# Kernel tuning notes

Hardware: AMD Instinct MI355X
Metric: run time of the kernel (lower is better)

Reference implementation:

```python
import jax, jax.numpy as jnp
import numpy as np

N, E, D = 50000, 800000, 128

def setup_inputs() -> dict:
    key = jax.random.key(0)
    ks = jax.random.split(key, 8)
    s = 0.02
    x = jax.random.normal(ks[0], (N, D), dtype=jnp.float32)
    edge_index = jax.random.randint(ks[1], (2, E), 0, N, dtype=jnp.int64)
    Wn = jax.random.normal(ks[2], (D, D), dtype=jnp.float32) * s
    bn = jax.random.normal(ks[3], (D,), dtype=jnp.float32) * s
    We = jax.random.normal(ks[4], (D, 2 * D), dtype=jnp.float32) * s
    be = jax.random.normal(ks[5], (D,), dtype=jnp.float32) * s
    Wu = jax.random.normal(ks[6], (D, 3 * D), dtype=jnp.float32) * s
    bu = jax.random.normal(ks[7], (D,), dtype=jnp.float32) * s
    return {"x": x, "edge_index": edge_index, "Wn": Wn, "bn": bn,
            "We": We, "be": be, "Wu": Wu, "bu": bu}

def reference(x, edge_index, Wn, bn, We, be, Wu, bu):
    n = x.shape[0]
    # 1. per-node linear transform (torch Linear: x @ W.T + b)
    node = x @ Wn.T + bn                                   # [N, D]
    src, dst = edge_index[0], edge_index[1]
    # 2. per-edge embedding from concatenated endpoint node embeddings
    edge_in = jnp.concatenate([node[src], node[dst]], axis=1)  # [E, 2D]
    edge_emb = edge_in @ We.T + be                          # [E, D]
    # 3. scatter-sum neighbor node embeddings and incident edge embeddings to src vertex
    nbr_sum = jax.ops.segment_sum(node[dst], src, num_segments=n)    # [N, D]
    edge_sum = jax.ops.segment_sum(edge_emb, src, num_segments=n)   # [N, D]
    pre_gelu = jnp.concatenate([node, nbr_sum, edge_sum], axis=1)    # [N, 3D]
    # 4-5. GELU (exact, matching torch nn.GELU default) + final linear
    out = jax.nn.gelu(pre_gelu, approximate=False) @ Wu.T + bu       # [N, D]
    return out
```

## Files before the change

### kernel.cpp

```cpp
#include <hip/hip_runtime.h>
#include <hip/hip_bf16.h>
#include <math.h>

typedef __attribute__((ext_vector_type(8))) short short8;
typedef __attribute__((ext_vector_type(4))) float f32x4;

#define CAP8 16

__device__ __forceinline__ float bf2f(unsigned short u) {
    union { unsigned int i; float f; } c; c.i = ((unsigned int)u) << 16; return c.f;
}
__device__ __forceinline__ unsigned short f2bf(float f) {
    __hip_bfloat16 h = __float2bfloat16(f);
    union { __hip_bfloat16 h; unsigned short u; } c; c.h = h; return c.u;
}
__device__ __forceinline__ float gelu_exact(float x) {
    return 0.5f * x * (1.0f + erff(x * 0.7071067811865475f));
}
__device__ __forceinline__ short8 ldcvt8(const float* p) {
    float4 f0 = *(const float4*)p;
    float4 f1 = *(const float4*)(p + 4);
    short8 a;
    a[0] = (short)f2bf(f0.x); a[1] = (short)f2bf(f0.y);
    a[2] = (short)f2bf(f0.z); a[3] = (short)f2bf(f0.w);
    a[4] = (short)f2bf(f1.x); a[5] = (short)f2bf(f1.y);
    a[6] = (short)f2bf(f1.z); a[7] = (short)f2bf(f1.w);
    return a;
}
__device__ __forceinline__ int swz(int row, int colbyte) {
    return row * 256 + (colbyte ^ ((row & 7) << 4));
}

__device__ __forceinline__ int detect_flag(const int* ei, int E) {
    int orv = 0;
    int lim = (E < 64) ? E : 64;
    for (int i = 0; i < lim; i++) orv |= ei[2 * i + 1];
    return (orv == 0) ? 1 : 0;
}
__device__ __forceinline__ int ld_src(const int* ei, int flag, int E, int e) {
    return flag ? ei[2 * (size_t)e] : ei[e];
}
__device__ __forceinline__ int ld_dst(const int* ei, int flag, int E, int e) {
    return flag ? ei[2 * (size_t)(E + e)] : ei[E + e];
}

__device__ __forceinline__ void gemm1_body(int bid,
                                           const float* __restrict__ x,
                                           const float* __restrict__ Wn,
                                           const float* __restrict__ bias,
                                           unsigned short* __restrict__ node,
                                           unsigned short* __restrict__ Apre0,
                                           int N) {
    const int v0 = bid * 64;
    const int wave = threadIdx.x >> 6;
    const int lane = threadIdx.x & 63;
    const int m    = lane & 15;
    const int kq   = lane >> 4;

    short8 B[2][4];
#pragma unroll
    for (int ntl = 0; ntl < 2; ntl++) {
        const int j = (wave * 2 + ntl) * 16 + m;
#pragma unroll
        for (int kb = 0; kb < 4; kb++)
            B[ntl][kb] = ldcvt8(Wn + (size_t)j * 128 + kb * 32 + kq * 8);
    }

    f32x4 acc[4][2];
#pragma unroll
    for (int mt = 0; mt < 4; mt++)
#pragma unroll
        for (int ntl = 0; ntl < 2; ntl++) acc[mt][ntl] = (f32x4){0.f,0.f,0.f,0.f};

#pragma unroll
    for (int kb = 0; kb < 4; kb++) {
#pragma unroll
        for (int mt = 0; mt < 4; mt++) {
            const int row = v0 + mt * 16 + m;
            short8 a = (short8){0,0,0,0,0,0,0,0};
            if (row < N) a = ldcvt8(x + (size_t)row * 128 + kb * 32 + kq * 8);
#pragma unroll
            for (int ntl = 0; ntl < 2; ntl++)
                acc[mt][ntl] = __builtin_amdgcn_mfma_f32_16x16x32_bf16(a, B[ntl][kb], acc[mt][ntl], 0, 0, 0);
        }
    }

    const int ocol = lane & 15;
#pragma unroll
    for (int mt = 0; mt < 4; mt++) {
#pragma unroll
        for (int ntl = 0; ntl < 2; ntl++) {
            const int col = (wave * 2 + ntl) * 16 + ocol;
            const float bval = bias[col];
#pragma unroll
            for (int r = 0; r < 4; r++) {
                const int row = v0 + mt * 16 + (lane >> 4) * 4 + r;
                if (row < N) {
                    const float v = acc[mt][ntl][r] + bval;
                    node[(size_t)row * 128 + col]  = f2bf(v);
                    Apre0[(size_t)row * 128 + col] = f2bf(gelu_exact(v));
                }
            }
        }
    }
}

__launch_bounds__(256)
__global__ void fused_a(const float* __restrict__ x,
                        const float* __restrict__ Wn,
                        const float* __restrict__ bn,
                        unsigned short* __restrict__ node,
                        unsigned short* __restrict__ Apre0,
                        const int* __restrict__ ei,
                        int* __restrict__ cursor8,
                        unsigned short* __restrict__ csr8,
                        int E, int N, int mblocks) {
    const int grp = blockIdx.x >> 3;
    if ((grp % 5) == 2) {
        const int mid = ((grp - 2) / 5) * 8 + (int)(blockIdx.x & 7);
        if (mid < mblocks) gemm1_body(mid, x, Wn, bn, node, Apre0, N);
        return;
    }
    __shared__ int sflag;
    if (threadIdx.x == 0) sflag = detect_flag(ei, E);
    __syncthreads();
    const int fgrp = grp - (grp + 2) / 5;
    const int e = (fgrp * 8 + (int)(blockIdx.x & 7)) * 256 + (int)threadIdx.x;
    if (e >= E) return;
    const int s = ld_src(ei, sflag, E, e);
    const int d = ld_dst(ei, sflag, E, e);
    if ((unsigned)s >= (unsigned)N || (unsigned)d >= (unsigned)N) return;
    const int b = (int)(blockIdx.x & 7);
    const int p = atomicAdd(&cursor8[(size_t)b * N + s], 1);
    if (p < CAP8) csr8[(size_t)s * 128 + b * CAP8 + p] = (unsigned short)d;
}

__launch_bounds__(256)
__global__ void gather_kernel(const int* __restrict__ cursor8,
                              const unsigned short* __restrict__ csr8,
                              const unsigned short* __restrict__ node,
                              unsigned short* __restrict__ nbr,
                              unsigned short* __restrict__ gnbr,
                              int N) {
    __shared__ int degB[8][8];
    const int v0 = blockIdx.x * 8;
    const int tid = threadIdx.x;
    if (tid < 64) {
        const int b = tid >> 3, vi = tid & 7;
        const int v = v0 + vi;
        int c = (v < N) ? cursor8[(size_t)b * N + v] : 0;
        degB[vi][b] = (c > CAP8) ? CAP8 : c;
    }
    __syncthreads();

    const int vl = tid >> 5;
    const int p  = (tid >> 4) & 1;
    const int c  = (tid & 15) * 8;
    const int v  = v0 + vl;

    float acc[8] = {0.f,0.f,0.f,0.f,0.f,0.f,0.f,0.f};
    if (v < N) {
        const unsigned short* __restrict__ vbase = csr8 + (size_t)v * 128;
#pragma unroll
        for (int bi = 0; bi < 4; bi++) {
            const int b = bi * 2 + p;
            const int cnt = degB[vl][b];
            const unsigned short* base = vbase + b * CAP8;
            int j = 0;
            for (; j + 2 <= cnt; j += 2) {
                const int i0 = base[j], i1 = base[j + 1];
                short8 a0 = *(const short8*)(node + (size_t)i0 * 128 + c);
                short8 a1 = *(const short8*)(node + (size_t)i1 * 128 + c);
#pragma unroll
                for (int k = 0; k < 8; k++)
                    acc[k] += bf2f((unsigned short)a0[k]) + bf2f((unsigned short)a1[k]);
            }
            if (j < cnt) {
                const int i0 = base[j];
                short8 a0 = *(const short8*)(node + (size_t)i0 * 128 + c);
#pragma unroll
                for (int k = 0; k < 8; k++) acc[k] += bf2f((unsigned short)a0[k]);
            }
        }
    }
#pragma unroll
    for (int k = 0; k < 8; k++) acc[k] += __shfl_xor(acc[k], 16);

    if (v < N) {
        short8 o;
        if (p == 0) {
#pragma unroll
            for (int k = 0; k < 8; k++) o[k] = (short)f2bf(acc[k]);
            *(short8*)(nbr + (size_t)v * 128 + c) = o;
        } else {
#pragma unroll
            for (int k = 0; k < 8; k++) o[k] = (short)f2bf(gelu_exact(acc[k]));
            *(short8*)(gnbr + (size_t)v * 128 + c) = o;
        }
    }
}

__launch_bounds__(256)
__global__ void gemm23_kernel(const int* __restrict__ cursor8,
                              const unsigned short* __restrict__ node,
                              const unsigned short* __restrict__ nbr,
                              const unsigned short* __restrict__ gnbr,
                              const unsigned short* __restrict__ Apre0,
                              const float* __restrict__ We,
                              const float* __restrict__ be,
                              const float* __restrict__ Wu,
                              const float* __restrict__ bu,
                              float* __restrict__ out, int N) {
    __shared__ unsigned short p2T[64 * 128];
    __shared__ float degT[64];

    const int v0   = blockIdx.x * 64;
    const int tid  = threadIdx.x;
    const int wave = tid >> 6;
    const int lane = tid & 63;
    const int m    = lane & 15;
    const int kq   = lane >> 4;

    if (tid < 64) {
        const int v = v0 + tid;
        int s = 0;
        if (v < N) {
#pragma unroll
            for (int b = 0; b < 8; b++) {
                int c = cursor8[(size_t)b * N + v];
                s += (c > CAP8) ? CAP8 : c;
            }
        }
        degT[tid] = (float)s;
    }
    __syncthreads();

    {
        short8 B[2][4][2];
#pragma unroll
        for (int ntl = 0; ntl < 2; ntl++) {
            const int j = (wave * 2 + ntl) * 16 + m;
#pragma unroll
            for (int kb = 0; kb < 4; kb++)
#pragma unroll
                for (int s = 0; s < 2; s++)
                    B[ntl][kb][s] = ldcvt8(We + (size_t)j * 256 + s * 128 + kb * 32 + kq * 8);
        }

        f32x4 acc2[4][2];
#pragma unroll
        for (int mt = 0; mt < 4; mt++)
#pragma unroll
            for (int ntl = 0; ntl < 2; ntl++) acc2[mt][ntl] = (f32x4){0.f,0.f,0.f,0.f};

#pragma unroll
        for (int kb = 0; kb < 4; kb++) {
#pragma unroll
            for (int mt = 0; mt < 4; mt++) {
                const int lrow = mt * 16 + m;
                const int row  = v0 + lrow;
                short8 an = (short8){0,0,0,0,0,0,0,0};
                short8 ab = an;
                if (row < N) {
                    an = *(const short8*)(node + (size_t)row * 128 + kb * 32 + kq * 8);
                    ab = *(const short8*)(nbr  + (size_t)row * 128 + kb * 32 + kq * 8);
                    const float dg = degT[lrow];
#pragma unroll
                    for (int k = 0; k < 8; k++)
                        an[k] = (short)f2bf(dg * bf2f((unsigned short)an[k]));
                }
#pragma unroll
                for (int ntl = 0; ntl < 2; ntl++) {
                    acc2[mt][ntl] = __builtin_amdgcn_mfma_f32_16x16x32_bf16(an, B[ntl][kb][0], acc2[mt][ntl], 0, 0, 0);
                    acc2[mt][ntl] = __builtin_amdgcn_mfma_f32_16x16x32_bf16(ab, B[ntl][kb][1], acc2[mt][ntl], 0, 0, 0);
                }
            }
        }

        const int ocol = lane & 15;
#pragma unroll
        for (int mt = 0; mt < 4; mt++) {
#pragma unroll
            for (int ntl = 0; ntl < 2; ntl++) {
                const int col = (wave * 2 + ntl) * 16 + ocol;
                const float bval = be[col];
#pragma unroll
                for (int r = 0; r < 4; r++) {
                    const int lrow = mt * 16 + (lane >> 4) * 4 + r;
                    const float dg = degT[lrow];
                    const float vv = gelu_exact(acc2[mt][ntl][r] + dg * bval);
                    *(unsigned short*)((char*)p2T + swz(lrow, col * 2)) = f2bf(vv);
                }
            }
        }
    }
    __syncthreads();

    {
        f32x4 acc3[4][2];
#pragma unroll
        for (int mt = 0; mt < 4; mt++)
#pragma unroll
            for (int ntl = 0; ntl < 2; ntl++) acc3[mt][ntl] = (f32x4){0.f,0.f,0.f,0.f};

#pragma unroll
        for (int s = 0; s < 3; s++) {
            short8 B3[2][4];
#pragma unroll
            for (int ntl = 0; ntl < 2; ntl++) {
                const int j = (wave * 2 + ntl) * 16 + m;
#pragma unroll
                for (int kb = 0; kb < 4; kb++)
                    B3[ntl][kb] = ldcvt8(Wu + (size_t)j * 384 + s * 128 + kb * 32 + kq * 8);
            }
#pragma unroll
            for (int kb = 0; kb < 4; kb++) {
#pragma unroll
                for (int mt = 0; mt < 4; mt++) {
                    const int lrow = mt * 16 + m;
                    const int row  = v0 + lrow;
                    short8 a = (short8){0,0,0,0,0,0,0,0};
                    if (s == 0) {
                        if (row < N) a = *(const short8*)(Apre0 + (size_t)row * 128 + kb * 32 + kq * 8);
                    } else if (s == 1) {
                        if (row < N) a = *(const short8*)(gnbr + (size_t)row * 128 + kb * 32 + kq * 8);
                    } else {
                        a = *(const short8*)((const char*)p2T + swz(lrow, kb * 64 + kq * 16));
                    }
#pragma unroll
                    for (int ntl = 0; ntl < 2; ntl++)
                        acc3[mt][ntl] = __builtin_amdgcn_mfma_f32_16x16x32_bf16(a, B3[ntl][kb], acc3[mt][ntl], 0, 0, 0);
                }
            }
        }

        const int ocol = lane & 15;
#pragma unroll
        for (int mt = 0; mt < 4; mt++) {
#pragma unroll
            for (int ntl = 0; ntl < 2; ntl++) {
                const int col = (wave * 2 + ntl) * 16 + ocol;
                const float bval = bu[col];
#pragma unroll
                for (int r = 0; r < 4; r++) {
                    const int row = v0 + mt * 16 + (lane >> 4) * 4 + r;
                    if (row < N)
                        out[(size_t)row * 128 + col] = acc3[mt][ntl][r] + bval;
                }
            }
        }
    }
}

extern "C" void kernel_launch(void* const* d_in, const int* in_sizes, int n_in,
                              void* d_out, int out_size, void* d_ws, size_t ws_size,
                              hipStream_t stream) {
    const float* x  = (const float*)d_in[0];
    const int*   ei = (const int*)d_in[1];
    const float* Wn = (const float*)d_in[2];
    const float* bn = (const float*)d_in[3];
    const float* We = (const float*)d_in[4];
    const float* be = (const float*)d_in[5];
    const float* Wu = (const float*)d_in[6];
    const float* bu = (const float*)d_in[7];

    const int N = in_sizes[0] / 128;
    const int E = in_sizes[1] / 2;

    char* ws = (char*)d_ws;
    size_t off = 0;
    unsigned short* node  = (unsigned short*)(ws + off); off += (size_t)N * 128 * 2;
    unsigned short* Apre0 = (unsigned short*)(ws + off); off += (size_t)N * 128 * 2;
    unsigned short* nbr   = (unsigned short*)(ws + off); off += (size_t)N * 128 * 2;
    unsigned short* gnbr  = (unsigned short*)(ws + off); off += (size_t)N * 128 * 2;
    off = (off + 255) & ~(size_t)255;
    int* cursor8 = (int*)(ws + off);                     off += (size_t)8 * N * 4;
    off = (off + 255) & ~(size_t)255;
    unsigned short* csr8 = (unsigned short*)(ws + off);  off += (size_t)N * 8 * CAP8 * 2;

    hipMemsetAsync(cursor8, 0, (size_t)8 * N * 4, stream);

    const int mblocks = (N + 63) / 64;
    const int eblocks = (E + 255) / 256;
    const int fgroups = (eblocks + 7) / 8;
    const int ggroups = (mblocks + 7) / 8;
    const int tgroups = fgroups + ggroups;
    const int grid_a  = tgroups * 8;

    fused_a<<<grid_a, 256, 0, stream>>>(x, Wn, bn, node, Apre0, ei, cursor8, csr8, E, N, mblocks);
    gather_kernel<<<(N + 7) / 8, 256, 0, stream>>>(cursor8, csr8, node, nbr, gnbr, N);
    gemm23_kernel<<<mblocks, 256, 0, stream>>>(cursor8, node, nbr, gnbr, Apre0, We, be, Wu, bu, (float*)d_out, N);
}
```

Measured before the change: 275.6 us.

## Pre-convert weights to bf16, compact per-node neighbor lists, shrink GEMM tile

Adds an init kernel that zeroes the cursor array, replacing the memset, and converts Wn, We and Wu to bf16 once so the GEMM blocks load pre-converted weights instead of converting them per block. The gather kernel now gives one wave per node: it compacts the eight bucketed CSR slots into a shared-memory list with ballot and popcount, then issues four independent row loads per step. The edge/update GEMM kernel uses 32-row tiles instead of 64 and loads weights per k-step rather than holding them all in registers, which raises block count and lowers register pressure. The edge-index loads become int2 vector loads. The costs are an extra kernel launch and more redundant weight loads per output row.

```diff
diff --git a/kernel.cpp b/kernel.cpp
--- a/kernel.cpp
+++ b/kernel.cpp
@@ -38,15 +38,31 @@
     return (orv == 0) ? 1 : 0;
 }
 __device__ __forceinline__ int ld_src(const int* ei, int flag, int E, int e) {
-    return flag ? ei[2 * (size_t)e] : ei[e];
+    if (flag) { int2 p = *(const int2*)(ei + 2 * (size_t)e); return p.x; }
+    return ei[e];
 }
 __device__ __forceinline__ int ld_dst(const int* ei, int flag, int E, int e) {
-    return flag ? ei[2 * (size_t)(E + e)] : ei[E + e];
+    if (flag) { int2 p = *(const int2*)(ei + 2 * (size_t)(E + e)); return p.x; }
+    return ei[E + e];
+}
+
+__launch_bounds__(256)
+__global__ void init_kernel(const float* __restrict__ Wn, const float* __restrict__ We,
+                            const float* __restrict__ Wu,
+                            unsigned short* __restrict__ Wnb, unsigned short* __restrict__ Web,
+                            unsigned short* __restrict__ Wub,
+                            int* __restrict__ cursor8, int N) {
+    const int stride = gridDim.x * 256;
+    const int t = blockIdx.x * 256 + threadIdx.x;
+    for (int i = t; i < 8 * N; i += stride) cursor8[i] = 0;
+    for (int i = t; i < 128 * 128; i += stride) Wnb[i] = f2bf(Wn[i]);
+    for (int i = t; i < 128 * 256; i += stride) Web[i] = f2bf(We[i]);
+    for (int i = t; i < 128 * 384; i += stride) Wub[i] = f2bf(Wu[i]);
 }
 
 __device__ __forceinline__ void gemm1_body(int bid,
                                            const float* __restrict__ x,
-                                           const float* __restrict__ Wn,
+                                           const unsigned short* __restrict__ Wnb,
                                            const float* __restrict__ bias,
                                            unsigned short* __restrict__ node,
                                            unsigned short* __restrict__ Apre0,
@@ -63,7 +79,7 @@
         const int j = (wave * 2 + ntl) * 16 + m;
 #pragma unroll
         for (int kb = 0; kb < 4; kb++)
-            B[ntl][kb] = ldcvt8(Wn + (size_t)j * 128 + kb * 32 + kq * 8);
+            B[ntl][kb] = *(const short8*)(Wnb + (size_t)j * 128 + kb * 32 + kq * 8);
     }
 
     f32x4 acc[4][2];
@@ -107,7 +123,7 @@
 
 __launch_bounds__(256)
 __global__ void fused_a(const float* __restrict__ x,
-                        const float* __restrict__ Wn,
+                        const unsigned short* __restrict__ Wnb,
                         const float* __restrict__ bn,
                         unsigned short* __restrict__ node,
                         unsigned short* __restrict__ Apre0,
@@ -118,7 +134,7 @@
     const int grp = blockIdx.x >> 3;
     if ((grp % 5) == 2) {
         const int mid = ((grp - 2) / 5) * 8 + (int)(blockIdx.x & 7);
-        if (mid < mblocks) gemm1_body(mid, x, Wn, bn, node, Apre0, N);
+        if (mid < mblocks) gemm1_body(mid, x, Wnb, bn, node, Apre0, N);
         return;
     }
     __shared__ int sflag;
@@ -142,61 +158,65 @@
                               unsigned short* __restrict__ nbr,
                               unsigned short* __restrict__ gnbr,
                               int N) {
-    __shared__ int degB[8][8];
-    const int v0 = blockIdx.x * 8;
-    const int tid = threadIdx.x;
-    if (tid < 64) {
-        const int b = tid >> 3, vi = tid & 7;
-        const int v = v0 + vi;
-        int c = (v < N) ? cursor8[(size_t)b * N + v] : 0;
-        degB[vi][b] = (c > CAP8) ? CAP8 : c;
-    }
-    __syncthreads();
-
-    const int vl = tid >> 5;
-    const int p  = (tid >> 4) & 1;
-    const int c  = (tid & 15) * 8;
-    const int v  = v0 + vl;
+    __shared__ unsigned short list[4][128];
+    const int tid  = threadIdx.x;
+    const int wave = tid >> 6;
+    const int lane = tid & 63;
+    const int way  = lane >> 4;
+    const int sl   = lane & 15;
+    const int v    = blockIdx.x * 4 + wave;
+    if (v >= N) return;
+
+    const int slot0 = lane, slot1 = lane + 64;
+    int c0 = cursor8[(size_t)(slot0 >> 4) * N + v]; if (c0 > CAP8) c0 = CAP8;
+    int c1 = cursor8[(size_t)(slot1 >> 4) * N + v]; if (c1 > CAP8) c1 = CAP8;
+    const unsigned short i0 = csr8[(size_t)v * 128 + slot0];
+    const unsigned short i1 = csr8[(size_t)v * 128 + slot1];
+    const bool vd0 = (slot0 & 15) < c0;
+    const bool vd1 = (slot1 & 15) < c1;
+    const unsigned long long m0 = __ballot(vd0);
+    const unsigned long long m1 = __ballot(vd1);
+    const unsigned long long below = (lane == 63) ? 0x7fffffffffffffffull
+                                                  : ((1ull << lane) - 1ull);
+    const int n0 = __popcll(m0);
+    if (vd0) list[wave][__popcll(m0 & below)] = i0;
+    if (vd1) list[wave][n0 + __popcll(m1 & below)] = i1;
+    const int deg = n0 + __popcll(m1);
+    asm volatile("s_waitcnt lgkmcnt(0)" ::: "memory");
 
     float acc[8] = {0.f,0.f,0.f,0.f,0.f,0.f,0.f,0.f};
-    if (v < N) {
-        const unsigned short* __restrict__ vbase = csr8 + (size_t)v * 128;
-#pragma unroll
-        for (int bi = 0; bi < 4; bi++) {
-            const int b = bi * 2 + p;
-            const int cnt = degB[vl][b];
-            const unsigned short* base = vbase + b * CAP8;
-            int j = 0;
-            for (; j + 2 <= cnt; j += 2) {
-                const int i0 = base[j], i1 = base[j + 1];
-                short8 a0 = *(const short8*)(node + (size_t)i0 * 128 + c);
-                short8 a1 = *(const short8*)(node + (size_t)i1 * 128 + c);
-#pragma unroll
-                for (int k = 0; k < 8; k++)
-                    acc[k] += bf2f((unsigned short)a0[k]) + bf2f((unsigned short)a1[k]);
-            }
-            if (j < cnt) {
-                const int i0 = base[j];
-                short8 a0 = *(const short8*)(node + (size_t)i0 * 128 + c);
-#pragma unroll
-                for (int k = 0; k < 8; k++) acc[k] += bf2f((unsigned short)a0[k]);
-            }
-        }
-    }
-#pragma unroll
-    for (int k = 0; k < 8; k++) acc[k] += __shfl_xor(acc[k], 16);
-
-    if (v < N) {
+    for (int base = 0; base < deg; base += 16) {
+        short8 a[4];
+        int r[4];
+#pragma unroll
+        for (int u = 0; u < 4; u++) {
+            r[u] = base + way + u * 4;
+            const unsigned short id = (r[u] < deg) ? list[wave][r[u]] : (unsigned short)0;
+            a[u] = *(const short8*)(node + (size_t)id * 128 + sl * 8);
+        }
+#pragma unroll
+        for (int u = 0; u < 4; u++) {
+            if (r[u] < deg) {
+#pragma unroll
+                for (int k = 0; k < 8; k++) acc[k] += bf2f((unsigned short)a[u][k]);
+            }
+        }
+    }
+#pragma unroll
+    for (int k = 0; k < 8; k++) {
+        acc[k] += __shfl_xor(acc[k], 16);
+        acc[k] += __shfl_xor(acc[k], 32);
+    }
+    if (way == 0) {
         short8 o;
-        if (p == 0) {
-#pragma unroll
-            for (int k = 0; k < 8; k++) o[k] = (short)f2bf(acc[k]);
-            *(short8*)(nbr + (size_t)v * 128 + c) = o;
-        } else {
-#pragma unroll
-            for (int k = 0; k < 8; k++) o[k] = (short)f2bf(gelu_exact(acc[k]));
-            *(short8*)(gnbr + (size_t)v * 128 + c) = o;
-        }
+#pragma unroll
+        for (int k = 0; k < 8; k++) o[k] = (short)f2bf(acc[k]);
+        *(short8*)(nbr + (size_t)v * 128 + sl * 8) = o;
+    } else if (way == 1) {
+        short8 o;
+#pragma unroll
+        for (int k = 0; k < 8; k++) o[k] = (short)f2bf(gelu_exact(acc[k]));
+        *(short8*)(gnbr + (size_t)v * 128 + sl * 8) = o;
     }
 }
 
@@ -206,22 +226,23 @@
                               const unsigned short* __restrict__ nbr,
                               const unsigned short* __restrict__ gnbr,
                               const unsigned short* __restrict__ Apre0,
-                              const float* __restrict__ We,
+                              const unsigned short* __restrict__ Web,
                               const float* __restrict__ be,
-                              const float* __restrict__ Wu,
+                              const unsigned short* __restrict__ Wub,
                               const float* __restrict__ bu,
                               float* __restrict__ out, int N) {
-    __shared__ unsigned short p2T[64 * 128];
-    __shared__ float degT[64];
-
-    const int v0   = blockIdx.x * 64;
+    __shared__ unsigned short p2T[32 * 128];
+    __shared__ float degT[32];
+
+    const int v0   = blockIdx.x * 32;
     const int tid  = threadIdx.x;
     const int wave = tid >> 6;
     const int lane = tid & 63;
     const int m    = lane & 15;
     const int kq   = lane >> 4;
-
-    if (tid < 64) {
+    const bool full = (v0 + 32 <= N);
+
+    if (tid < 32) {
         const int v = v0 + tid;
         int s = 0;
         if (v < N) {
@@ -236,50 +257,51 @@
     __syncthreads();
 
     {
-        short8 B[2][4][2];
-#pragma unroll
-        for (int ntl = 0; ntl < 2; ntl++) {
-            const int j = (wave * 2 + ntl) * 16 + m;
-#pragma unroll
-            for (int kb = 0; kb < 4; kb++)
-#pragma unroll
-                for (int s = 0; s < 2; s++)
-                    B[ntl][kb][s] = ldcvt8(We + (size_t)j * 256 + s * 128 + kb * 32 + kq * 8);
-        }
-
-        f32x4 acc2[4][2];
-#pragma unroll
-        for (int mt = 0; mt < 4; mt++)
+        f32x4 acc2[2][2];
+#pragma unroll
+        for (int mt = 0; mt < 2; mt++)
 #pragma unroll
             for (int ntl = 0; ntl < 2; ntl++) acc2[mt][ntl] = (f32x4){0.f,0.f,0.f,0.f};
 
 #pragma unroll
         for (int kb = 0; kb < 4; kb++) {
-#pragma unroll
-            for (int mt = 0; mt < 4; mt++) {
-                const int lrow = mt * 16 + m;
-                const int row  = v0 + lrow;
-                short8 an = (short8){0,0,0,0,0,0,0,0};
-                short8 ab = an;
-                if (row < N) {
-                    an = *(const short8*)(node + (size_t)row * 128 + kb * 32 + kq * 8);
-                    ab = *(const short8*)(nbr  + (size_t)row * 128 + kb * 32 + kq * 8);
-                    const float dg = degT[lrow];
-#pragma unroll
-                    for (int k = 0; k < 8; k++)
-                        an[k] = (short)f2bf(dg * bf2f((unsigned short)an[k]));
-                }
+            short8 B0[2], B1[2], an[2], ab[2];
+#pragma unroll
+            for (int ntl = 0; ntl < 2; ntl++) {
+                const int j = (wave * 2 + ntl) * 16 + m;
+                B0[ntl] = *(const short8*)(Web + (size_t)j * 256 + kb * 32 + kq * 8);
+                B1[ntl] = *(const short8*)(Web + (size_t)j * 256 + 128 + kb * 32 + kq * 8);
+            }
+#pragma unroll
+            for (int mt = 0; mt < 2; mt++) {
+                const int row = v0 + mt * 16 + m;
+                if (full || row < N) {
+                    an[mt] = *(const short8*)(node + (size_t)row * 128 + kb * 32 + kq * 8);
+                    ab[mt] = *(const short8*)(nbr  + (size_t)row * 128 + kb * 32 + kq * 8);
+                } else {
+                    an[mt] = (short8){0,0,0,0,0,0,0,0};
+                    ab[mt] = (short8){0,0,0,0,0,0,0,0};
+                }
+            }
+#pragma unroll
+            for (int mt = 0; mt < 2; mt++) {
+                const float dg = degT[mt * 16 + m];
+#pragma unroll
+                for (int k = 0; k < 8; k++)
+                    an[mt][k] = (short)f2bf(dg * bf2f((unsigned short)an[mt][k]));
+            }
+#pragma unroll
+            for (int mt = 0; mt < 2; mt++)
 #pragma unroll
                 for (int ntl = 0; ntl < 2; ntl++) {
-                    acc2[mt][ntl] = __builtin_amdgcn_mfma_f32_16x16x32_bf16(an, B[ntl][kb][0], acc2[mt][ntl], 0, 0, 0);
-                    acc2[mt][ntl] = __builtin_amdgcn_mfma_f32_16x16x32_bf16(ab, B[ntl][kb][1], acc2[mt][ntl], 0, 0, 0);
-                }
-            }
+                    acc2[mt][ntl] = __builtin_amdgcn_mfma_f32_16x16x32_bf16(an[mt], B0[ntl], acc2[mt][ntl], 0, 0, 0);
+                    acc2[mt][ntl] = __builtin_amdgcn_mfma_f32_16x16x32_bf16(ab[mt], B1[ntl], acc2[mt][ntl], 0, 0, 0);
+                }
         }
 
         const int ocol = lane & 15;
 #pragma unroll
-        for (int mt = 0; mt < 4; mt++) {
+        for (int mt = 0; mt < 2; mt++) {
 #pragma unroll
             for (int ntl = 0; ntl < 2; ntl++) {
                 const int col = (wave * 2 + ntl) * 16 + ocol;
@@ -297,46 +319,47 @@
     __syncthreads();
 
     {
-        f32x4 acc3[4][2];
-#pragma unroll
-        for (int mt = 0; mt < 4; mt++)
+        f32x4 acc3[2][2];
+#pragma unroll
+        for (int mt = 0; mt < 2; mt++)
 #pragma unroll
             for (int ntl = 0; ntl < 2; ntl++) acc3[mt][ntl] = (f32x4){0.f,0.f,0.f,0.f};
 
 #pragma unroll
         for (int s = 0; s < 3; s++) {
-            short8 B3[2][4];
-#pragma unroll
-            for (int ntl = 0; ntl < 2; ntl++) {
-                const int j = (wave * 2 + ntl) * 16 + m;
-#pragma unroll
-                for (int kb = 0; kb < 4; kb++)
-                    B3[ntl][kb] = ldcvt8(Wu + (size_t)j * 384 + s * 128 + kb * 32 + kq * 8);
-            }
 #pragma unroll
             for (int kb = 0; kb < 4; kb++) {
-#pragma unroll
-                for (int mt = 0; mt < 4; mt++) {
+                short8 B3[2], a[2];
+#pragma unroll
+                for (int ntl = 0; ntl < 2; ntl++) {
+                    const int j = (wave * 2 + ntl) * 16 + m;
+                    B3[ntl] = *(const short8*)(Wub + (size_t)j * 384 + s * 128 + kb * 32 + kq * 8);
+                }
+#pragma unroll
+                for (int mt = 0; mt < 2; mt++) {
                     const int lrow = mt * 16 + m;
                     const int row  = v0 + lrow;
-                    short8 a = (short8){0,0,0,0,0,0,0,0};
                     if (s == 0) {
-                        if (row < N) a = *(const short8*)(Apre0 + (size_t)row * 128 + kb * 32 + kq * 8);
+                        a[mt] = (full || row < N) ? *(const short8*)(Apre0 + (size_t)row * 128 + kb * 32 + kq * 8)
+                                                  : (short8){0,0,0,0,0,0,0,0};
                     } else if (s == 1) {
-                        if (row < N) a = *(const short8*)(gnbr + (size_t)row * 128 + kb * 32 + kq * 8);
+                        a[mt] = (full || row < N) ? *(const short8*)(gnbr + (size_t)row * 128 + kb * 32 + kq * 8)
+                                                  : (short8){0,0,0,0,0,0,0,0};
                     } else {
-                        a = *(const short8*)((const char*)p2T + swz(lrow, kb * 64 + kq * 16));
+                        a[mt] = *(const short8*)((const char*)p2T + swz(lrow, kb * 64 + kq * 16));
                     }
+                }
+#pragma unroll
+                for (int mt = 0; mt < 2; mt++)
 #pragma unroll
                     for (int ntl = 0; ntl < 2; ntl++)
-                        acc3[mt][ntl] = __builtin_amdgcn_mfma_f32_16x16x32_bf16(a, B3[ntl][kb], acc3[mt][ntl], 0, 0, 0);
-                }
+                        acc3[mt][ntl] = __builtin_amdgcn_mfma_f32_16x16x32_bf16(a[mt], B3[ntl], acc3[mt][ntl], 0, 0, 0);
             }
         }
 
         const int ocol = lane & 15;
 #pragma unroll
-        for (int mt = 0; mt < 4; mt++) {
+        for (int mt = 0; mt < 2; mt++) {
 #pragma unroll
             for (int ntl = 0; ntl < 2; ntl++) {
                 const int col = (wave * 2 + ntl) * 16 + ocol;
@@ -377,8 +400,10 @@
     int* cursor8 = (int*)(ws + off);                     off += (size_t)8 * N * 4;
     off = (off + 255) & ~(size_t)255;
     unsigned short* csr8 = (unsigned short*)(ws + off);  off += (size_t)N * 8 * CAP8 * 2;
-
-    hipMemsetAsync(cursor8, 0, (size_t)8 * N * 4, stream);
+    off = (off + 255) & ~(size_t)255;
+    unsigned short* Wnb = (unsigned short*)(ws + off);   off += (size_t)128 * 128 * 2;
+    unsigned short* Web = (unsigned short*)(ws + off);   off += (size_t)128 * 256 * 2;
+    unsigned short* Wub = (unsigned short*)(ws + off);   off += (size_t)128 * 384 * 2;
 
     const int mblocks = (N + 63) / 64;
     const int eblocks = (E + 255) / 256;
@@ -387,7 +412,8 @@
     const int tgroups = fgroups + ggroups;
     const int grid_a  = tgroups * 8;
 
-    fused_a<<<grid_a, 256, 0, stream>>>(x, Wn, bn, node, Apre0, ei, cursor8, csr8, E, N, mblocks);
-    gather_kernel<<<(N + 7) / 8, 256, 0, stream>>>(cursor8, csr8, node, nbr, gnbr, N);
-    gemm23_kernel<<<mblocks, 256, 0, stream>>>(cursor8, node, nbr, gnbr, Apre0, We, be, Wu, bu, (float*)d_out, N);
-}
+    init_kernel<<<512, 256, 0, stream>>>(Wn, We, Wu, Wnb, Web, Wub, cursor8, N);
+    fused_a<<<grid_a, 256, 0, stream>>>(x, Wnb, bn, node, Apre0, ei, cursor8, csr8, E, N, mblocks);
+    gather_kernel<<<(N + 3) / 4, 256, 0, stream>>>(cursor8, csr8, node, nbr, gnbr, N);
+    gemm23_kernel<<<(N + 31) / 32, 256, 0, stream>>>(cursor8, node, nbr, gnbr, Apre0, Web, be, Wub, bu, (float*)d_out, N);
+}
```

New measurement: 236.5 us. 14.2% less time.
